# Optimization experiments

Measured on AMD Instinct MI355X. Metric: run time of the kernel, lower is better.

The kernel has to match this reference:

```python
import jax, jax.numpy as jnp
import numpy as np

B, L, DH = 8, 512, 768
D_ARC, D_REL, C = 512, 128, 37


def setup_inputs() -> dict:
    key = jax.random.key(0)
    ks = jax.random.split(key, 14)
    n = jax.random.normal
    return {
        "H": n(ks[0], (B, L, DH), jnp.float32),
        "W_ah": n(ks[1], (D_ARC, DH), jnp.float32) * 0.02,
        "b_ah": n(ks[2], (D_ARC,), jnp.float32) * 0.02,
        "W_ad": n(ks[3], (D_ARC, DH), jnp.float32) * 0.02,
        "b_ad": n(ks[4], (D_ARC,), jnp.float32) * 0.02,
        "W_arc": n(ks[5], (D_ARC, D_ARC), jnp.float32) * 0.02,
        "bias_arc": n(ks[6], (D_ARC,), jnp.float32) * 0.02,
        "W_rh": n(ks[7], (D_REL, DH), jnp.float32) * 0.02,
        "b_rh": n(ks[8], (D_REL,), jnp.float32) * 0.02,
        "W_rd": n(ks[9], (D_REL, DH), jnp.float32) * 0.02,
        "b_rd": n(ks[10], (D_REL,), jnp.float32) * 0.02,
        "U_rel": n(ks[11], (C, D_REL, D_REL), jnp.float32) * 0.02,
        "W_rel": n(ks[12], (C, 2 * D_REL), jnp.float32) * 0.02,
        "bias_rel": n(ks[13], (C,), jnp.float32) * 0.02,
    }


def reference(H, W_ah, b_ah, W_ad, b_ad, W_arc, bias_arc,
              W_rh, b_rh, W_rd, b_rd, U_rel, W_rel, bias_rel):
    relu = jax.nn.relu
    # Arc path: MLPs (dropout is identity at inference)
    Hah = relu(H @ W_ah.T + b_ah)          # [B,L,d_arc] heads
    Had = relu(H @ W_ad.T + b_ad)          # [B,L,d_arc] deps
    # S_arc[b,l,m] = (Had W_arc^T)[b,l] . Hah[b,m] + Hah[b,l] . bias_arc
    S_arc = jnp.einsum('bld,bmd->blm', Had @ W_arc.T, Hah)
    S_arc = S_arc + (Hah @ bias_arc)[:, :, None]
    # Rel path
    Hrh = relu(H @ W_rh.T + b_rh)          # [B,L,d_rel]
    Hrd = relu(H @ W_rd.T + b_rd)          # [B,L,d_rel]
    # Bilinear per-label term: [B,L,L,C]
    bilin = jnp.einsum('bld,cde,bme->blmc', Hrh, U_rel, Hrd)
    # Affine term: faithful to the original expand — both head and dep are
    # taken at index l (expansion over dim 2), so it is independent of m.
    affine = jnp.concatenate([Hrh, Hrd], axis=-1) @ W_rel.T  # [B,L,C]
    S_rel = bilin + affine[:, :, None, :] + bias_rel
    return (S_arc, S_rel)
```

## Files before the change

### kernel.cpp

```cpp
#include <hip/hip_runtime.h>
#include <hip/hip_bf16.h>

typedef __attribute__((ext_vector_type(8))) short bf16x8;
typedef __attribute__((ext_vector_type(4))) float f32x4;

#define DEVINL __device__ __forceinline__

constexpr int kB = 8, kL = 512, kDH = 768, kDARC = 512, kDREL = 128, kC = 37;
constexpr int kBL = kB * kL;
constexpr int kNP = 1280;
constexpr int kNY = kC * kDREL;

constexpr long nHB   = (long)kBL * kDH;
constexpr long nWALL = (long)kNP * kDH;
constexpr long nWARC = (long)kDARC * kDARC;
constexpr long nUT   = (long)kC * kDREL * kDREL;
constexpr long nBALL = kNP;

DEVINL short f2b(float f) {
  unsigned u = __float_as_uint(f);
  u += 0x7fffu + ((u >> 16) & 1u);
  return (short)(u >> 16);
}
DEVINL float b2f(short s) {
  return __uint_as_float(((unsigned)(unsigned short)s) << 16);
}

DEVINL void gload16(const void* g, void* l) {
  __builtin_amdgcn_global_load_lds(
      (const __attribute__((address_space(1))) void*)g,
      (__attribute__((address_space(3))) void*)l, 16, 0, 0);
}

__global__ __launch_bounds__(256) void k_convert(
    const float* __restrict__ H, const float* __restrict__ W_ah, const float* __restrict__ b_ah,
    const float* __restrict__ W_ad, const float* __restrict__ b_ad,
    const float* __restrict__ W_arc, const float* __restrict__ W_rh, const float* __restrict__ b_rh,
    const float* __restrict__ W_rd, const float* __restrict__ b_rd, const float* __restrict__ U,
    short* __restrict__ Hb, short* __restrict__ Wall, float* __restrict__ ballf,
    short* __restrict__ Warcb, short* __restrict__ Ut)
{
  const long total = nHB + nWALL + nWARC + nUT + nBALL;
  for (long i = (long)blockIdx.x * blockDim.x + threadIdx.x; i < total;
       i += (long)gridDim.x * blockDim.x) {
    if (i < nHB) {
      Hb[i] = f2b(H[i]);
    } else if (i < nHB + nWALL) {
      long j = i - nHB; int row = (int)(j / kDH); int k = (int)(j - (long)row * kDH);
      float v;
      if (row < 512)       v = W_ah[(long)row * kDH + k];
      else if (row < 1024) v = W_ad[(long)(row - 512) * kDH + k];
      else if (row < 1152) v = W_rh[(long)(row - 1024) * kDH + k];
      else                 v = W_rd[(long)(row - 1152) * kDH + k];
      Wall[j] = f2b(v);
    } else if (i < nHB + nWALL + nWARC) {
      long j = i - nHB - nWALL;
      Warcb[j] = f2b(W_arc[j]);
    } else if (i < nHB + nWALL + nWARC + nUT) {
      long j = i - nHB - nWALL - nWARC;
      int c = (int)(j >> 14); int rem = (int)(j & 16383); int e = rem >> 7; int d = rem & 127;
      Ut[j] = f2b(U[(long)c * 16384 + (long)d * 128 + e]);
    } else {
      int n = (int)(i - nHB - nWALL - nWARC - nUT);
      float v;
      if (n < 512)       v = b_ah[n];
      else if (n < 1024) v = b_ad[n - 512];
      else if (n < 1152) v = b_rh[n - 1024];
      else               v = b_rd[n - 1152];
      ballf[n] = v;
    }
  }
}

DEVINL void gemm128_core(const short* __restrict__ Ag, long lda,
                         const short* __restrict__ Bg, long ldb,
                         int K, f32x4 acc[4][4])
{
  __shared__ short As[128 * 64];
  __shared__ short Bs[128 * 64];
  const int t = threadIdx.x, lane = t & 63, w = t >> 6;
  const int wm = w >> 1, wn = w & 1, fr = lane & 15, hi = lane >> 4;
  const int srow = w * 8 + (lane >> 3);
  const int scol = (lane & 7) * 8;
  const short* Arow = Ag + (long)srow * lda + scol;
  const short* Brow = Bg + (long)srow * ldb + scol;

  for (int k0 = 0; k0 < K; k0 += 64) {
    __syncthreads();
#pragma unroll
    for (int i = 0; i < 4; i++) {
      gload16(Arow + (long)i * 32 * lda + k0, &As[(i * 4 + w) * 512]);
      gload16(Brow + (long)i * 32 * ldb + k0, &Bs[(i * 4 + w) * 512]);
    }
    __syncthreads();
#pragma unroll
    for (int ks = 0; ks < 2; ks++) {
      bf16x8 a[4], b[4];
#pragma unroll
      for (int mf = 0; mf < 4; mf++)
        a[mf] = *(const bf16x8*)&As[(wm * 64 + mf * 16 + fr) * 64 + ks * 32 + hi * 8];
#pragma unroll
      for (int nf = 0; nf < 4; nf++)
        b[nf] = *(const bf16x8*)&Bs[(wn * 64 + nf * 16 + fr) * 64 + ks * 32 + hi * 8];
#pragma unroll
      for (int mf = 0; mf < 4; mf++)
#pragma unroll
        for (int nf = 0; nf < 4; nf++)
          acc[mf][nf] = __builtin_amdgcn_mfma_f32_16x16x32_bf16(a[mf], b[nf], acc[mf][nf], 0, 0, 0);
    }
  }
}

#define ZERO_ACC16 \
  f32x4 acc[4][4]; \
  for (int i = 0; i < 4; i++) for (int j = 0; j < 4; j++) for (int r = 0; r < 4; r++) acc[i][j][r] = 0.f;

__global__ __launch_bounds__(256) void k_proj(const short* __restrict__ Hb,
    const short* __restrict__ Wall, const float* __restrict__ ballf,
    short* __restrict__ Proj)
{
  const int tn = blockIdx.x, tm = blockIdx.y;
  ZERO_ACC16;
  gemm128_core(Hb + (long)tm * 128 * kDH, kDH, Wall + (long)tn * 128 * kDH, kDH, kDH, acc);
  const int lane = threadIdx.x & 63; const int w = threadIdx.x >> 6;
  const int wm = w >> 1, wn = w & 1, fr = lane & 15, hi = lane >> 4;
  for (int mf = 0; mf < 4; mf++) for (int nf = 0; nf < 4; nf++) for (int r = 0; r < 4; r++) {
    int row = tm * 128 + wm * 64 + mf * 16 + hi * 4 + r;
    int col = tn * 128 + wn * 64 + nf * 16 + fr;
    float v = acc[mf][nf][r] + ballf[col];
    v = v > 0.f ? v : 0.f;
    Proj[(long)row * kNP + col] = f2b(v);
  }
}

__global__ __launch_bounds__(256) void k_mid(const short* __restrict__ Proj,
    const short* __restrict__ Warcb, const short* __restrict__ Ut,
    const float* __restrict__ bias_arc, const float* __restrict__ W_rel,
    const float* __restrict__ bias_rel,
    short* __restrict__ T, short* __restrict__ Y,
    float* __restrict__ rowterm, float* __restrict__ affB)
{
  const int bx = blockIdx.x;
  const int t = threadIdx.x;
  __shared__ float h[4][256];

  if (bx < 1312) {
    const short* Ag; const short* Bg;
    long lda, ldb, ldd; int K, tm, tn; short* dst;
    if (bx < 128) {
      tn = bx & 3; tm = bx >> 2;
      Ag = Proj + (long)tm * 128 * kNP + 512; lda = kNP;
      Bg = Warcb + (long)tn * 128 * kDARC;    ldb = kDARC;
      K = kDARC; dst = T; ldd = kDARC;
    } else {
      int i = bx - 128; tn = i % 37; tm = i / 37;
      Ag = Proj + (long)tm * 128 * kNP + 1024; lda = kNP;
      Bg = Ut + (long)tn * 128 * kDREL;        ldb = kDREL;
      K = kDREL; dst = Y; ldd = kNY;
    }
    ZERO_ACC16;
    gemm128_core(Ag, lda, Bg, ldb, K, acc);
    const int lane = t & 63; const int w = t >> 6;
    const int wm = w >> 1, wn = w & 1, fr = lane & 15, hi = lane >> 4;
    for (int mf = 0; mf < 4; mf++) for (int nf = 0; nf < 4; nf++) for (int r = 0; r < 4; r++) {
      int row = tm * 128 + wm * 64 + mf * 16 + hi * 4 + r;
      int col = tn * 128 + wn * 64 + nf * 16 + fr;
      dst[(long)row * ldd + col] = f2b(acc[mf][nf][r]);
    }
  } else {
    const int base = (bx - 1312) * 8;
    const int w = t >> 6, lane = t & 63;
    for (int j = 0; j < 2; j++) {
      const int bl = base + w * 2 + j;
      const short* prow = Proj + (long)bl * kNP;
      float s = 0.f;
      bf16x8 hv = *(const bf16x8*)(prow + lane * 8);
#pragma unroll
      for (int i = 0; i < 8; i++) s += b2f(hv[i]) * bias_arc[lane * 8 + i];
      for (int off = 32; off; off >>= 1) s += __shfl_down(s, off, 64);
      if (lane == 0) rowterm[bl] = s;
      if (lane < 32) {
        bf16x8 v = *(const bf16x8*)(prow + 1024 + lane * 8);
        for (int i = 0; i < 8; i++) h[w][lane * 8 + i] = b2f(v[i]);
      }
      __syncthreads();
      if (lane < kC) {
        float sa = bias_rel[lane];
        const float* wr = W_rel + (long)lane * 256;
        for (int k = 0; k < 256; k++) sa += h[w][k] * wr[k];
        affB[(long)bl * kC + lane] = sa;
      }
      __syncthreads();
    }
  }
}

__global__ __launch_bounds__(512) void k_out(const short* __restrict__ T,
    const short* __restrict__ Proj, const float* __restrict__ rowterm,
    const short* __restrict__ Y, const float* __restrict__ affB,
    float* __restrict__ outArc, float* __restrict__ outRel)
{
  __shared__ short sm[24576];
  const int t = threadIdx.x;
  const int lane = t & 63, w = t >> 6;
  const int fr = lane & 15, hi = lane >> 4;

  if (blockIdx.x < 64) {
    const int i = blockIdx.x;
    const int b = i >> 3, tm = (i >> 2) & 1, tn = i & 3;
    const int wm = w >> 1, wn = w & 1;
    short* As = sm;
    short* Bs = sm + 16384;
    const short* Ag = T + ((long)b * kL + tm * 256) * kDARC;
    const short* Bg = Proj + ((long)b * kL + tn * 128) * kNP;
    const int sr8 = lane >> 3;
    const int sc = (lane & 7) * 8;
    const short* Arow = Ag + (long)(w * 8 + sr8) * kDARC + sc;
    const short* Brow = Bg + (long)(w * 8 + sr8) * kNP + sc;

    ZERO_ACC16;
    for (int k0 = 0; k0 < kDARC; k0 += 64) {
      __syncthreads();
#pragma unroll
      for (int i2 = 0; i2 < 4; i2++)
        gload16(Arow + (long)i2 * 64 * kDARC + k0, &As[(i2 * 64 + w * 8) * 64]);
#pragma unroll
      for (int i2 = 0; i2 < 2; i2++)
        gload16(Brow + (long)i2 * 64 * kNP + k0, &Bs[(i2 * 64 + w * 8) * 64]);
      __syncthreads();
#pragma unroll
      for (int ks = 0; ks < 2; ks++) {
        bf16x8 a[4], bb[4];
#pragma unroll
        for (int mf = 0; mf < 4; mf++)
          a[mf] = *(const bf16x8*)&As[(wm * 64 + mf * 16 + fr) * 64 + ks * 32 + hi * 8];
#pragma unroll
        for (int nf = 0; nf < 4; nf++)
          bb[nf] = *(const bf16x8*)&Bs[(wn * 64 + nf * 16 + fr) * 64 + ks * 32 + hi * 8];
#pragma unroll
        for (int mf = 0; mf < 4; mf++)
#pragma unroll
          for (int nf = 0; nf < 4; nf++)
            acc[mf][nf] = __builtin_amdgcn_mfma_f32_16x16x32_bf16(a[mf], bb[nf], acc[mf][nf], 0, 0, 0);
      }
    }
    for (int mf = 0; mf < 4; mf++) for (int nf = 0; nf < 4; nf++) for (int r = 0; r < 4; r++) {
      int l = tm * 256 + wm * 64 + mf * 16 + hi * 4 + r;
      int m = tn * 128 + wn * 64 + nf * 16 + fr;
      outArc[((long)b * kL + l) * kL + m] = acc[mf][nf][r] + rowterm[(long)b * kL + l];
    }
  } else {
    const int i = blockIdx.x - 64;
    const int b = i >> 6;
    const int l0 = (i & 63) * 8;
    short* Bcur = sm;
    short* Bnxt = sm + 6528;

    if (t < 352) {
      int buf = t / 176, q = t % 176;
      int c = 37 + (q >> 4), e = (q & 15) * 8;
      bf16x8 z = {0, 0, 0, 0, 0, 0, 0, 0};
      *(bf16x8*)&sm[buf * 6528 + c * 136 + e] = z;
    }

    bf16x8 a[4][4];
    const short* Ab = Proj + ((long)b * kL + w * 64) * kNP + 1152;
#pragma unroll
    for (int mf = 0; mf < 4; mf++)
#pragma unroll
      for (int ks = 0; ks < 4; ks++)
        a[mf][ks] = *(const bf16x8*)(Ab + (long)(mf * 16 + fr) * kNP + ks * 32 + hi * 8);

    {
      const short* Yrow = Y + ((long)b * kL + l0) * kNY;
      bf16x8 s0 = *(const bf16x8*)(Yrow + t * 8);
      *(bf16x8*)&Bcur[(t >> 4) * 136 + (t & 15) * 8] = s0;
      if (t < 80) {
        int c2 = 512 + t;
        bf16x8 s1 = *(const bf16x8*)(Yrow + (long)c2 * 8);
        *(bf16x8*)&Bcur[(c2 >> 4) * 136 + (c2 & 15) * 8] = s1;
      }
    }
    __syncthreads();

    for (int il = 0; il < 8; il++) {
      const long bl = (long)b * kL + l0 + il;

      bf16x8 n0, n1;
      if (il < 7) {
        const short* Yn = Y + (bl + 1) * kNY;
        n0 = *(const bf16x8*)(Yn + t * 8);
        if (t < 80) n1 = *(const bf16x8*)(Yn + (long)(512 + t) * 8);
      }

      f32x4 acc[4][3];
#pragma unroll
      for (int mf = 0; mf < 4; mf++)
#pragma unroll
        for (int nf = 0; nf < 3; nf++)
          for (int r = 0; r < 4; r++) acc[mf][nf][r] = 0.f;

#pragma unroll
      for (int ks = 0; ks < 4; ks++) {
        bf16x8 bfr[3];
#pragma unroll
        for (int nf = 0; nf < 3; nf++)
          bfr[nf] = *(const bf16x8*)&Bcur[(nf * 16 + fr) * 136 + ks * 32 + hi * 8];
#pragma unroll
        for (int mf = 0; mf < 4; mf++)
#pragma unroll
          for (int nf = 0; nf < 3; nf++)
            acc[mf][nf] = __builtin_amdgcn_mfma_f32_16x16x32_bf16(a[mf][ks], bfr[nf], acc[mf][nf], 0, 0, 0);
      }

      if (il < 7) {
        *(bf16x8*)&Bnxt[(t >> 4) * 136 + (t & 15) * 8] = n0;
        if (t < 80) {
          int c2 = 512 + t;
          *(bf16x8*)&Bnxt[(c2 >> 4) * 136 + (c2 & 15) * 8] = n1;
        }
        __syncthreads();
        short* tmp = Bcur; Bcur = Bnxt; Bnxt = tmp;
      }

      float* ob = outRel + (bl * kL + w * 64) * kC;
      const float* afb = affB + bl * kC;
#pragma unroll
      for (int nf = 0; nf < 3; nf++) {
        int c = nf * 16 + fr;
        if (c < kC) {
          float aff = afb[c];
#pragma unroll
          for (int mf = 0; mf < 4; mf++)
            for (int r = 0; r < 4; r++)
              ob[(long)(mf * 16 + hi * 4 + r) * kC + c] = acc[mf][nf][r] + aff;
        }
      }
    }
  }
}

extern "C" void kernel_launch(void* const* d_in, const int* in_sizes, int n_in,
                              void* d_out, int out_size, void* d_ws, size_t ws_size,
                              hipStream_t stream) {
  const float* H        = (const float*)d_in[0];
  const float* W_ah     = (const float*)d_in[1];
  const float* b_ah     = (const float*)d_in[2];
  const float* W_ad     = (const float*)d_in[3];
  const float* b_ad     = (const float*)d_in[4];
  const float* W_arc    = (const float*)d_in[5];
  const float* bias_arc = (const float*)d_in[6];
  const float* W_rh     = (const float*)d_in[7];
  const float* b_rh     = (const float*)d_in[8];
  const float* W_rd     = (const float*)d_in[9];
  const float* b_rd     = (const float*)d_in[10];
  const float* U_rel    = (const float*)d_in[11];
  const float* W_rel    = (const float*)d_in[12];
  const float* bias_rel = (const float*)d_in[13];

  size_t off = 0;
  auto take = [&](size_t nbytes) -> void* {
    void* p = (char*)d_ws + off;
    off += (nbytes + 255) & ~(size_t)255;
    return p;
  };
  short* Hb      = (short*)take(nHB * 2);
  short* Wall    = (short*)take(nWALL * 2);
  float* ballf   = (float*)take(nBALL * 4);
  short* Warcb   = (short*)take(nWARC * 2);
  short* Ut      = (short*)take(nUT * 2);
  short* Proj    = (short*)take((long)kBL * kNP * 2);
  short* T       = (short*)take((long)kBL * kDARC * 2);
  short* Y       = (short*)take((long)kBL * kNY * 2);
  float* rowterm = (float*)take((long)kBL * 4);
  float* affB    = (float*)take((long)kBL * kC * 4);
  if (off > ws_size) return;

  float* outArc = (float*)d_out;
  float* outRel = outArc + (long)kB * kL * kL;

  k_convert<<<dim3(2048), dim3(256), 0, stream>>>(H, W_ah, b_ah, W_ad, b_ad, W_arc,
                                                  W_rh, b_rh, W_rd, b_rd, U_rel,
                                                  Hb, Wall, ballf, Warcb, Ut);
  k_proj<<<dim3(kNP / 128, kBL / 128), dim3(256), 0, stream>>>(Hb, Wall, ballf, Proj);
  k_mid<<<dim3(1824), dim3(256), 0, stream>>>(Proj, Warcb, Ut, bias_arc, W_rel, bias_rel,
                                              T, Y, rowterm, affB);
  k_out<<<dim3(576), dim3(512), 0, stream>>>(T, Proj, rowterm, Y, affB, outArc, outRel);
}
```

Before: 191.3 us.

## Stage rel-score tiles through LDS for coalesced stores and split k_out blocks

The output kernel now runs 256 threads per block, with twice as many blocks. The arc GEMM reuses the shared 128x128 gemm core, and each rel block covers half of the m range. Rel scores are first written into an LDS scratch area, which reuses the current B buffer after a barrier. They are then stored to global memory as contiguous float4 vectors instead of strided scalar writes. The change targets uncoalesced 37-stride output stores and tries to improve occupancy. In exchange it adds an extra barrier per row and reloads the Proj A fragments in twice as many blocks.

```diff
diff --git a/kernel.cpp b/kernel.cpp
--- a/kernel.cpp
+++ b/kernel.cpp
@@ -72,12 +72,11 @@
   }
 }
 
-DEVINL void gemm128_core(const short* __restrict__ Ag, long lda,
+DEVINL void gemm128_core(short* As, short* Bs,
+                         const short* __restrict__ Ag, long lda,
                          const short* __restrict__ Bg, long ldb,
                          int K, f32x4 acc[4][4])
 {
-  __shared__ short As[128 * 64];
-  __shared__ short Bs[128 * 64];
   const int t = threadIdx.x, lane = t & 63, w = t >> 6;
   const int wm = w >> 1, wn = w & 1, fr = lane & 15, hi = lane >> 4;
   const int srow = w * 8 + (lane >> 3);
@@ -119,9 +118,10 @@
     const short* __restrict__ Wall, const float* __restrict__ ballf,
     short* __restrict__ Proj)
 {
+  __shared__ short As[128 * 64], Bs[128 * 64];
   const int tn = blockIdx.x, tm = blockIdx.y;
   ZERO_ACC16;
-  gemm128_core(Hb + (long)tm * 128 * kDH, kDH, Wall + (long)tn * 128 * kDH, kDH, kDH, acc);
+  gemm128_core(As, Bs, Hb + (long)tm * 128 * kDH, kDH, Wall + (long)tn * 128 * kDH, kDH, kDH, acc);
   const int lane = threadIdx.x & 63; const int w = threadIdx.x >> 6;
   const int wm = w >> 1, wn = w & 1, fr = lane & 15, hi = lane >> 4;
   for (int mf = 0; mf < 4; mf++) for (int nf = 0; nf < 4; nf++) for (int r = 0; r < 4; r++) {
@@ -140,9 +140,9 @@
     short* __restrict__ T, short* __restrict__ Y,
     float* __restrict__ rowterm, float* __restrict__ affB)
 {
+  __shared__ short As[128 * 64], Bs[128 * 64];
   const int bx = blockIdx.x;
   const int t = threadIdx.x;
-  __shared__ float h[4][256];
 
   if (bx < 1312) {
     const short* Ag; const short* Bg;
@@ -159,7 +159,7 @@
       K = kDREL; dst = Y; ldd = kNY;
     }
     ZERO_ACC16;
-    gemm128_core(Ag, lda, Bg, ldb, K, acc);
+    gemm128_core(As, Bs, Ag, lda, Bg, ldb, K, acc);
     const int lane = t & 63; const int w = t >> 6;
     const int wm = w >> 1, wn = w & 1, fr = lane & 15, hi = lane >> 4;
     for (int mf = 0; mf < 4; mf++) for (int nf = 0; nf < 4; nf++) for (int r = 0; r < 4; r++) {
@@ -168,6 +168,7 @@
       dst[(long)row * ldd + col] = f2b(acc[mf][nf][r]);
     }
   } else {
+    __shared__ float h[4][256];
     const int base = (bx - 1312) * 8;
     const int w = t >> 6, lane = t & 63;
     for (int j = 0; j < 2; j++) {
@@ -195,76 +196,40 @@
   }
 }
 
-__global__ __launch_bounds__(512) void k_out(const short* __restrict__ T,
+__global__ __launch_bounds__(256) void k_out(const short* __restrict__ T,
     const short* __restrict__ Proj, const float* __restrict__ rowterm,
     const short* __restrict__ Y, const float* __restrict__ affB,
     float* __restrict__ outArc, float* __restrict__ outRel)
 {
-  __shared__ short sm[24576];
+  extern __shared__ short sm[];
   const int t = threadIdx.x;
   const int lane = t & 63, w = t >> 6;
   const int fr = lane & 15, hi = lane >> 4;
 
-  if (blockIdx.x < 64) {
+  if (blockIdx.x < 128) {
     const int i = blockIdx.x;
-    const int b = i >> 3, tm = (i >> 2) & 1, tn = i & 3;
+    const int b = i >> 4, tm = (i >> 2) & 3, tn = i & 3;
+    ZERO_ACC16;
+    gemm128_core(sm, sm + 8192,
+                 T + ((long)b * kL + tm * 128) * kDARC, kDARC,
+                 Proj + ((long)b * kL + tn * 128) * kNP, kNP, kDARC, acc);
     const int wm = w >> 1, wn = w & 1;
-    short* As = sm;
-    short* Bs = sm + 16384;
-    const short* Ag = T + ((long)b * kL + tm * 256) * kDARC;
-    const short* Bg = Proj + ((long)b * kL + tn * 128) * kNP;
-    const int sr8 = lane >> 3;
-    const int sc = (lane & 7) * 8;
-    const short* Arow = Ag + (long)(w * 8 + sr8) * kDARC + sc;
-    const short* Brow = Bg + (long)(w * 8 + sr8) * kNP + sc;
-
-    ZERO_ACC16;
-    for (int k0 = 0; k0 < kDARC; k0 += 64) {
-      __syncthreads();
-#pragma unroll
-      for (int i2 = 0; i2 < 4; i2++)
-        gload16(Arow + (long)i2 * 64 * kDARC + k0, &As[(i2 * 64 + w * 8) * 64]);
-#pragma unroll
-      for (int i2 = 0; i2 < 2; i2++)
-        gload16(Brow + (long)i2 * 64 * kNP + k0, &Bs[(i2 * 64 + w * 8) * 64]);
-      __syncthreads();
-#pragma unroll
-      for (int ks = 0; ks < 2; ks++) {
-        bf16x8 a[4], bb[4];
-#pragma unroll
-        for (int mf = 0; mf < 4; mf++)
-          a[mf] = *(const bf16x8*)&As[(wm * 64 + mf * 16 + fr) * 64 + ks * 32 + hi * 8];
-#pragma unroll
-        for (int nf = 0; nf < 4; nf++)
-          bb[nf] = *(const bf16x8*)&Bs[(wn * 64 + nf * 16 + fr) * 64 + ks * 32 + hi * 8];
-#pragma unroll
-        for (int mf = 0; mf < 4; mf++)
-#pragma unroll
-          for (int nf = 0; nf < 4; nf++)
-            acc[mf][nf] = __builtin_amdgcn_mfma_f32_16x16x32_bf16(a[mf], bb[nf], acc[mf][nf], 0, 0, 0);
-      }
-    }
     for (int mf = 0; mf < 4; mf++) for (int nf = 0; nf < 4; nf++) for (int r = 0; r < 4; r++) {
-      int l = tm * 256 + wm * 64 + mf * 16 + hi * 4 + r;
+      int l = tm * 128 + wm * 64 + mf * 16 + hi * 4 + r;
       int m = tn * 128 + wn * 64 + nf * 16 + fr;
       outArc[((long)b * kL + l) * kL + m] = acc[mf][nf][r] + rowterm[(long)b * kL + l];
     }
   } else {
-    const int i = blockIdx.x - 64;
-    const int b = i >> 6;
-    const int l0 = (i & 63) * 8;
+    const int idx = blockIdx.x - 128;
+    const int h = idx & 1;
+    const int l0 = ((idx >> 1) & 63) * 8;
+    const int b = idx >> 7;
+    const int mbase = h * 256;
     short* Bcur = sm;
     short* Bnxt = sm + 6528;
 
-    if (t < 352) {
-      int buf = t / 176, q = t % 176;
-      int c = 37 + (q >> 4), e = (q & 15) * 8;
-      bf16x8 z = {0, 0, 0, 0, 0, 0, 0, 0};
-      *(bf16x8*)&sm[buf * 6528 + c * 136 + e] = z;
-    }
-
     bf16x8 a[4][4];
-    const short* Ab = Proj + ((long)b * kL + w * 64) * kNP + 1152;
+    const short* Ab = Proj + ((long)b * kL + mbase + w * 64) * kNP + 1152;
 #pragma unroll
     for (int mf = 0; mf < 4; mf++)
 #pragma unroll
@@ -273,12 +238,11 @@
 
     {
       const short* Yrow = Y + ((long)b * kL + l0) * kNY;
-      bf16x8 s0 = *(const bf16x8*)(Yrow + t * 8);
-      *(bf16x8*)&Bcur[(t >> 4) * 136 + (t & 15) * 8] = s0;
-      if (t < 80) {
-        int c2 = 512 + t;
-        bf16x8 s1 = *(const bf16x8*)(Yrow + (long)c2 * 8);
-        *(bf16x8*)&Bcur[(c2 >> 4) * 136 + (c2 & 15) * 8] = s1;
+#pragma unroll
+      for (int p = 0; p < 3; p++) {
+        int i2 = p * 256 + t;
+        if (i2 < 592)
+          *(bf16x8*)&Bcur[(i2 >> 4) * 136 + (i2 & 15) * 8] = *(const bf16x8*)(Yrow + i2 * 8);
       }
     }
     __syncthreads();
@@ -286,11 +250,12 @@
     for (int il = 0; il < 8; il++) {
       const long bl = (long)b * kL + l0 + il;
 
-      bf16x8 n0, n1;
+      bf16x8 n0, n1, n2;
       if (il < 7) {
         const short* Yn = Y + (bl + 1) * kNY;
         n0 = *(const bf16x8*)(Yn + t * 8);
-        if (t < 80) n1 = *(const bf16x8*)(Yn + (long)(512 + t) * 8);
+        n1 = *(const bf16x8*)(Yn + (long)(256 + t) * 8);
+        if (t < 80) n2 = *(const bf16x8*)(Yn + (long)(512 + t) * 8);
       }
 
       f32x4 acc[4][3];
@@ -312,29 +277,50 @@
           for (int nf = 0; nf < 3; nf++)
             acc[mf][nf] = __builtin_amdgcn_mfma_f32_16x16x32_bf16(a[mf][ks], bfr[nf], acc[mf][nf], 0, 0, 0);
       }
+      __syncthreads();
+
+      float aff[3];
+#pragma unroll
+      for (int nf = 0; nf < 3; nf++) {
+        int c = nf * 16 + fr;
+        aff[nf] = (c < kC) ? affB[bl * kC + c] : 0.f;
+      }
+
+      float* scr = (float*)Bcur + w * 592;
+#pragma unroll
+      for (int mf = 0; mf < 4; mf++) {
+#pragma unroll
+        for (int nf = 0; nf < 3; nf++) {
+          int c = nf * 16 + fr;
+          if (c < kC) {
+#pragma unroll
+            for (int r = 0; r < 4; r++)
+              scr[(hi * 4 + r) * kC + c] = acc[mf][nf][r] + aff[nf];
+          }
+        }
+        float* gb = outRel + (bl * kL + mbase + w * 64 + mf * 16) * kC;
+#pragma unroll
+        for (int p = 0; p < 3; p++) {
+          int i4 = p * 64 + lane;
+          if (i4 < 148) {
+            f32x4 v = *(f32x4*)&scr[i4 * 4];
+            *(f32x4*)&gb[i4 * 4] = v;
+          }
+        }
+      }
 
       if (il < 7) {
         *(bf16x8*)&Bnxt[(t >> 4) * 136 + (t & 15) * 8] = n0;
+        {
+          int i2 = 256 + t;
+          *(bf16x8*)&Bnxt[(i2 >> 4) * 136 + (i2 & 15) * 8] = n1;
+        }
         if (t < 80) {
-          int c2 = 512 + t;
-          *(bf16x8*)&Bnxt[(c2 >> 4) * 136 + (c2 & 15) * 8] = n1;
+          int i2 = 512 + t;
+          *(bf16x8*)&Bnxt[(i2 >> 4) * 136 + (i2 & 15) * 8] = n2;
         }
         __syncthreads();
         short* tmp = Bcur; Bcur = Bnxt; Bnxt = tmp;
-      }
-
-      float* ob = outRel + (bl * kL + w * 64) * kC;
-      const float* afb = affB + bl * kC;
-#pragma unroll
-      for (int nf = 0; nf < 3; nf++) {
-        int c = nf * 16 + fr;
-        if (c < kC) {
-          float aff = afb[c];
-#pragma unroll
-          for (int mf = 0; mf < 4; mf++)
-            for (int r = 0; r < 4; r++)
-              ob[(long)(mf * 16 + hi * 4 + r) * kC + c] = acc[mf][nf][r] + aff;
-        }
       }
     }
   }
@@ -385,5 +371,5 @@
   k_proj<<<dim3(kNP / 128, kBL / 128), dim3(256), 0, stream>>>(Hb, Wall, ballf, Proj);
   k_mid<<<dim3(1824), dim3(256), 0, stream>>>(Proj, Warcb, Ut, bias_arc, W_rel, bias_rel,
                                               T, Y, rowterm, affB);
-  k_out<<<dim3(576), dim3(512), 0, stream>>>(T, Proj, rowterm, Y, affB, outArc, outRel);
-}
+  k_out<<<dim3(1152), dim3(256), 32768, stream>>>(T, Proj, rowterm, Y, affB, outArc, outRel);
+}
```

New measurement: 161.0 us. -15.8%, faster.
